# Performance work log

Measured on AMD Instinct MI355X. Metric: run time of the kernel, lower is better.

Reference implementation:

```python
import jax, jax.numpy as jnp
import numpy as np

H = 4      # num_heads
C = 64     # attention_num_c
C_Z = 128  # num_in_c (pair rep channels)
C_T = 64   # num_in_c_kv (template pair channels)


def setup_inputs() -> dict:
    key = jax.random.key(0)
    ks = jax.random.split(key, 7)
    B, T, R = 1, 4, 384
    z2d = jax.random.normal(ks[0], (B, R, R, C_Z), dtype=jnp.float32)
    t2d = jax.random.normal(ks[1], (B, T, R, R, C_T), dtype=jnp.float32)
    s = 0.02
    Wq = jax.random.normal(ks[2], (C_Z, H * C), dtype=jnp.float32) * s
    Wk = jax.random.normal(ks[3], (C_T, H * C), dtype=jnp.float32) * s
    Wv = jax.random.normal(ks[4], (C_T, H * C), dtype=jnp.float32) * s
    Wo = jax.random.normal(ks[5], (H * C, C_Z), dtype=jnp.float32) * s
    bo = jax.random.normal(ks[6], (C_Z,), dtype=jnp.float32) * s
    return {"z2d": z2d, "t2d": t2d, "Wq": Wq, "Wk": Wk, "Wv": Wv, "Wo": Wo, "bo": bo}


def reference(z2d, t2d, Wq, Wk, Wv, Wo, bo):
    B, R = z2d.shape[0], z2d.shape[-2]
    T = t2d.shape[1]
    P = R * R  # residue-pair axis
    # query: one query per residue pair
    zq = z2d.reshape(B, P, 1, C_Z)
    # templates become the key/value axis per residue pair
    tkv = jnp.transpose(t2d, (0, 2, 3, 1, 4)).reshape(B, P, T, C_T)
    q = (zq @ Wq).reshape(B, P, 1, H, C) * (C ** -0.5)
    k = (tkv @ Wk).reshape(B, P, T, H, C)
    v = (tkv @ Wv).reshape(B, P, T, H, C)
    logits = jnp.einsum('bpqhc,bpkhc->bphqk', q, k)  # [B,P,H,1,T]
    weights = jax.nn.softmax(logits, axis=-1)
    weighted_avg = jnp.einsum('bphqk,bpkhc->bpqhc', weights, v)  # [B,P,1,H,C]
    out = weighted_avg.reshape(B, P, 1, H * C) @ Wo + bo
    return out.reshape(B, R, R, C_Z)
```

## Files before the change

### kernel.cpp

```cpp
#include <hip/hip_runtime.h>


#define R_   384
#define P_   (R_ * R_)
#define NBLK (P_ / 64)

typedef __attribute__((ext_vector_type(8))) short  short8;
typedef __attribute__((ext_vector_type(4))) float  f32x4;

__device__ __forceinline__ unsigned short f2bf(float f) {
  unsigned u = __float_as_uint(f);
  unsigned r = ((u >> 16) & 1u) + 0x7FFFu;
  return (unsigned short)((u + r) >> 16);
}
__device__ __forceinline__ float bf2f(unsigned short s) {
  return __uint_as_float(((unsigned)s) << 16);
}
__device__ __forceinline__ int swz(int p, int c) {
  return p * 256 + ((((c >> 3) ^ (p & 31)) << 3) | (c & 7));
}

__global__ void prep_kernel(const float* __restrict__ Wq, const float* __restrict__ Wk,
                            const float* __restrict__ Wv, const float* __restrict__ Wo,
                            unsigned short* __restrict__ AbarT,
                            unsigned short* __restrict__ MbarT) {
  int tid = blockIdx.x * blockDim.x + threadIdx.x;
  if (tid < 256 * 128) {
    int n = tid >> 7, i = tid & 127;
    int h = n >> 6, j = n & 63;
    const float* wq = Wq + i * 256 + h * 64;
    const float* wk = Wk + j * 256 + h * 64;
    float acc = 0.f;
#pragma unroll 8
    for (int c = 0; c < 64; ++c) acc += wq[c] * wk[c];
    AbarT[n * 128 + i] = f2bf(acc * 0.125f);
  } else {
    int t2 = tid - 256 * 128;
    int o = t2 >> 8, k = t2 & 255;
    int h = k >> 6, j = k & 63;
    const float* wv = Wv + j * 256 + h * 64;
    const float* wo = Wo + (h * 64) * 128 + o;
    float acc = 0.f;
#pragma unroll 8
    for (int c = 0; c < 64; ++c) acc += wv[c] * wo[c * 128];
    MbarT[o * 256 + k] = f2bf(acc);
  }
}

__global__ __launch_bounds__(256, 2) void attn_kernel(
    const float* __restrict__ z2d, const float* __restrict__ t2d,
    const unsigned short* __restrict__ AbarT, const unsigned short* __restrict__ MbarT,
    const float* __restrict__ bo, float* __restrict__ out) {
  __shared__ __align__(16) unsigned short sT[64 * 256];
  __shared__ __align__(16) unsigned short sG[64 * 256];

  const int tid = threadIdx.x;
  const int P0  = blockIdx.x * 64;

#pragma unroll
  for (int it = 0; it < 16; ++it) {
    int f  = it * 256 + tid;
    int t  = f >> 10;
    int rr = f & 1023;
    int p  = rr >> 4;
    int j4 = (rr & 15) << 2;
    const float4 v = *(const float4*)(t2d + (size_t)(t * P_ + P0 + p) * 64 + j4);
    ushort4 pk;
    pk.x = f2bf(v.x); pk.y = f2bf(v.y); pk.z = f2bf(v.z); pk.w = f2bf(v.w);
    *(ushort4*)(sT + swz(p, t * 64 + j4)) = pk;
  }

  const int wv_  = tid >> 6;
  const int lane = tid & 63;
  const int l = lane & 15;
  const int q = lane >> 4;

  f32x4 acc[16];
#pragma unroll
  for (int i = 0; i < 16; ++i) acc[i] = f32x4{0.f, 0.f, 0.f, 0.f};
  const float* zrow = z2d + (size_t)(P0 + wv_ * 16 + l) * 128;
#pragma unroll
  for (int kk = 0; kk < 4; ++kk) {
    float4 za = *(const float4*)(zrow + kk * 32 + q * 8);
    float4 zb = *(const float4*)(zrow + kk * 32 + q * 8 + 4);
    short8 af;
    af[0] = (short)f2bf(za.x); af[1] = (short)f2bf(za.y);
    af[2] = (short)f2bf(za.z); af[3] = (short)f2bf(za.w);
    af[4] = (short)f2bf(zb.x); af[5] = (short)f2bf(zb.y);
    af[6] = (short)f2bf(zb.z); af[7] = (short)f2bf(zb.w);
    const unsigned short* bbase = AbarT + l * 128 + kk * 32 + q * 8;
#pragma unroll
    for (int nt = 0; nt < 16; ++nt) {
      short8 bf = *(const short8*)(bbase + nt * 2048);
      acc[nt] = __builtin_amdgcn_mfma_f32_16x16x32_bf16(af, bf, acc[nt], 0, 0, 0);
    }
  }
#pragma unroll
  for (int nt = 0; nt < 16; ++nt) {
    int c = nt * 16 + l;
#pragma unroll
    for (int r = 0; r < 4; ++r) {
      int p = wv_ * 16 + q * 4 + r;
      sG[swz(p, c)] = f2bf(acc[nt][r]);
    }
  }
  __syncthreads();

  {
    const int p = tid & 63;
    const int h = tid >> 6;
    float lg0 = 0.f, lg1 = 0.f, lg2 = 0.f, lg3 = 0.f;
#pragma unroll
    for (int jb = 0; jb < 64; jb += 4) {
      ushort4 g4 = *(const ushort4*)(sG + swz(p, h * 64 + jb));
      float g0 = bf2f(g4.x), g1 = bf2f(g4.y), g2 = bf2f(g4.z), g3 = bf2f(g4.w);
      ushort4 k0 = *(const ushort4*)(sT + swz(p, jb));
      ushort4 k1 = *(const ushort4*)(sT + swz(p, 64 + jb));
      ushort4 k2 = *(const ushort4*)(sT + swz(p, 128 + jb));
      ushort4 k3 = *(const ushort4*)(sT + swz(p, 192 + jb));
      lg0 += g0 * bf2f(k0.x) + g1 * bf2f(k0.y) + g2 * bf2f(k0.z) + g3 * bf2f(k0.w);
      lg1 += g0 * bf2f(k1.x) + g1 * bf2f(k1.y) + g2 * bf2f(k1.z) + g3 * bf2f(k1.w);
      lg2 += g0 * bf2f(k2.x) + g1 * bf2f(k2.y) + g2 * bf2f(k2.z) + g3 * bf2f(k2.w);
      lg3 += g0 * bf2f(k3.x) + g1 * bf2f(k3.y) + g2 * bf2f(k3.z) + g3 * bf2f(k3.w);
    }
    float mx = fmaxf(fmaxf(lg0, lg1), fmaxf(lg2, lg3));
    float e0 = __expf(lg0 - mx), e1 = __expf(lg1 - mx);
    float e2 = __expf(lg2 - mx), e3 = __expf(lg3 - mx);
    float inv = 1.f / (e0 + e1 + e2 + e3);
    e0 *= inv; e1 *= inv; e2 *= inv; e3 *= inv;
#pragma unroll
    for (int jb = 0; jb < 64; jb += 4) {
      ushort4 k0 = *(const ushort4*)(sT + swz(p, jb));
      ushort4 k1 = *(const ushort4*)(sT + swz(p, 64 + jb));
      ushort4 k2 = *(const ushort4*)(sT + swz(p, 128 + jb));
      ushort4 k3 = *(const ushort4*)(sT + swz(p, 192 + jb));
      ushort4 sv;
      sv.x = f2bf(e0 * bf2f(k0.x) + e1 * bf2f(k1.x) + e2 * bf2f(k2.x) + e3 * bf2f(k3.x));
      sv.y = f2bf(e0 * bf2f(k0.y) + e1 * bf2f(k1.y) + e2 * bf2f(k2.y) + e3 * bf2f(k3.y));
      sv.z = f2bf(e0 * bf2f(k0.z) + e1 * bf2f(k1.z) + e2 * bf2f(k2.z) + e3 * bf2f(k3.z));
      sv.w = f2bf(e0 * bf2f(k0.w) + e1 * bf2f(k1.w) + e2 * bf2f(k2.w) + e3 * bf2f(k3.w));
      *(ushort4*)(sG + swz(p, h * 64 + jb)) = sv;
    }
  }
  __syncthreads();

  f32x4 acc2[4][2];
#pragma unroll
  for (int mt = 0; mt < 4; ++mt) {
    acc2[mt][0] = f32x4{0.f, 0.f, 0.f, 0.f};
    acc2[mt][1] = f32x4{0.f, 0.f, 0.f, 0.f};
  }
#pragma unroll
  for (int kk = 0; kk < 8; ++kk) {
    const unsigned short* mb = MbarT + (size_t)(wv_ * 32 + l) * 256 + kk * 32 + q * 8;
    short8 b0 = *(const short8*)(mb);
    short8 b1 = *(const short8*)(mb + 16 * 256);
#pragma unroll
    for (int mt = 0; mt < 4; ++mt) {
      const int p  = mt * 16 + l;
      const int cb = kk * 32 + q * 8;
      short8 af2 = *(const short8*)(sG + p * 256 + (((cb >> 3) ^ (p & 31)) << 3));
      acc2[mt][0] = __builtin_amdgcn_mfma_f32_16x16x32_bf16(af2, b0, acc2[mt][0], 0, 0, 0);
      acc2[mt][1] = __builtin_amdgcn_mfma_f32_16x16x32_bf16(af2, b1, acc2[mt][1], 0, 0, 0);
    }
  }
  const float bo0 = bo[wv_ * 32 + l];
  const float bo1 = bo[wv_ * 32 + 16 + l];
#pragma unroll
  for (int mt = 0; mt < 4; ++mt) {
#pragma unroll
    for (int r = 0; r < 4; ++r) {
      size_t row = (size_t)(P0 + mt * 16 + q * 4 + r);
      out[row * 128 + wv_ * 32 + l]      = acc2[mt][0][r] + bo0;
      out[row * 128 + wv_ * 32 + 16 + l] = acc2[mt][1][r] + bo1;
    }
  }
}

extern "C" void kernel_launch(void* const* d_in, const int* in_sizes, int n_in,
                              void* d_out, int out_size, void* d_ws, size_t ws_size,
                              hipStream_t stream) {
  const float* z2d = (const float*)d_in[0];
  const float* t2d = (const float*)d_in[1];
  const float* Wq  = (const float*)d_in[2];
  const float* Wk  = (const float*)d_in[3];
  const float* Wv  = (const float*)d_in[4];
  const float* Wo  = (const float*)d_in[5];
  const float* bo  = (const float*)d_in[6];

  unsigned short* AbarT = (unsigned short*)d_ws;
  unsigned short* MbarT = AbarT + 256 * 128;
  float* out = (float*)d_out;

  hipLaunchKernelGGL(prep_kernel, dim3(256), dim3(256), 0, stream,
                     Wq, Wk, Wv, Wo, AbarT, MbarT);
  hipLaunchKernelGGL(attn_kernel, dim3(NBLK), dim3(256), 0, stream,
                     z2d, t2d, AbarT, MbarT, bo, out);
}
```

Before: 358.3 us.

## Halve attention tile to 32 pairs, re-split waves, and rewrite weight prep with LDS

The attention kernel now processes 32 residue pairs per block instead of 64, halving shared memory and accumulator registers, and raises launch bounds to 4 blocks per CU. Waves are re-split into an M-tile by N-half grid for both MFMA GEMMs, and the logit/softmax stage splits each pair's channel reduction across two threads combined with a shuffle. The weight-folding prep kernel is rewritten to stage Wq/Wk/Wv/Wo slices in padded shared memory with 8 blocks instead of 256 strided-global-load blocks. The smaller tile increases redundant loads of the folded weight matrices per pair and doubles block count.

```diff
diff --git a/kernel.cpp b/kernel.cpp
--- a/kernel.cpp
+++ b/kernel.cpp
@@ -3,7 +3,7 @@
 
 #define R_   384
 #define P_   (R_ * R_)
-#define NBLK (P_ / 64)
+#define NBLK (P_ / 32)
 
 typedef __attribute__((ext_vector_type(8))) short  short8;
 typedef __attribute__((ext_vector_type(4))) float  f32x4;
@@ -24,44 +24,75 @@
                             const float* __restrict__ Wv, const float* __restrict__ Wo,
                             unsigned short* __restrict__ AbarT,
                             unsigned short* __restrict__ MbarT) {
-  int tid = blockIdx.x * blockDim.x + threadIdx.x;
-  if (tid < 256 * 128) {
-    int n = tid >> 7, i = tid & 127;
-    int h = n >> 6, j = n & 63;
-    const float* wq = Wq + i * 256 + h * 64;
-    const float* wk = Wk + j * 256 + h * 64;
-    float acc = 0.f;
+  __shared__ float sA[128 * 65];
+  __shared__ float sB[64 * 65];
+  const int t = threadIdx.x;
+  if (blockIdx.x < 4) {
+    const int h = blockIdx.x;
+    for (int it = 0; it < 8; ++it) {
+      int idx = it * 256 + t;
+      int row = idx >> 4, c4 = (idx & 15) << 2;
+      float4 v = *(const float4*)(Wq + row * 256 + h * 64 + c4);
+      sA[row * 65 + c4 + 0] = v.x; sA[row * 65 + c4 + 1] = v.y;
+      sA[row * 65 + c4 + 2] = v.z; sA[row * 65 + c4 + 3] = v.w;
+    }
+    for (int it = 0; it < 4; ++it) {
+      int idx = it * 256 + t;
+      int row = idx >> 4, c4 = (idx & 15) << 2;
+      float4 v = *(const float4*)(Wk + row * 256 + h * 64 + c4);
+      sB[row * 65 + c4 + 0] = v.x; sB[row * 65 + c4 + 1] = v.y;
+      sB[row * 65 + c4 + 2] = v.z; sB[row * 65 + c4 + 3] = v.w;
+    }
+    __syncthreads();
+    const int i = t & 127, jh2 = t >> 7;
+    for (int jj = 0; jj < 32; ++jj) {
+      int j = jh2 * 32 + jj;
+      float acc = 0.f;
 #pragma unroll 8
-    for (int c = 0; c < 64; ++c) acc += wq[c] * wk[c];
-    AbarT[n * 128 + i] = f2bf(acc * 0.125f);
+      for (int c = 0; c < 64; ++c) acc += sA[i * 65 + c] * sB[j * 65 + c];
+      AbarT[(h * 64 + j) * 128 + i] = f2bf(acc * 0.125f);
+    }
   } else {
-    int t2 = tid - 256 * 128;
-    int o = t2 >> 8, k = t2 & 255;
-    int h = k >> 6, j = k & 63;
-    const float* wv = Wv + j * 256 + h * 64;
-    const float* wo = Wo + (h * 64) * 128 + o;
-    float acc = 0.f;
+    const int h = blockIdx.x - 4;
+    for (int it = 0; it < 8; ++it) {
+      int idx = it * 256 + t;
+      int row = idx >> 5, o4 = (idx & 31) << 2;
+      *(float4*)(sA + row * 128 + o4) = *(const float4*)(Wo + (h * 64 + row) * 128 + o4);
+    }
+    for (int it = 0; it < 4; ++it) {
+      int idx = it * 256 + t;
+      int row = idx >> 4, c4 = (idx & 15) << 2;
+      float4 v = *(const float4*)(Wv + row * 256 + h * 64 + c4);
+      sB[row * 65 + c4 + 0] = v.x; sB[row * 65 + c4 + 1] = v.y;
+      sB[row * 65 + c4 + 2] = v.z; sB[row * 65 + c4 + 3] = v.w;
+    }
+    __syncthreads();
+    const int o = t & 127, jh2 = t >> 7;
+    for (int jj = 0; jj < 32; ++jj) {
+      int j = jh2 * 32 + jj;
+      float acc = 0.f;
 #pragma unroll 8
-    for (int c = 0; c < 64; ++c) acc += wv[c] * wo[c * 128];
-    MbarT[o * 256 + k] = f2bf(acc);
-  }
-}
-
-__global__ __launch_bounds__(256, 2) void attn_kernel(
+      for (int c = 0; c < 64; ++c) acc += sB[j * 65 + c] * sA[c * 128 + o];
+      MbarT[o * 256 + h * 64 + j] = f2bf(acc);
+    }
+  }
+}
+
+__global__ __launch_bounds__(256, 4) void attn_kernel(
     const float* __restrict__ z2d, const float* __restrict__ t2d,
     const unsigned short* __restrict__ AbarT, const unsigned short* __restrict__ MbarT,
     const float* __restrict__ bo, float* __restrict__ out) {
-  __shared__ __align__(16) unsigned short sT[64 * 256];
-  __shared__ __align__(16) unsigned short sG[64 * 256];
+  __shared__ __align__(16) unsigned short sT[32 * 256];
+  __shared__ __align__(16) unsigned short sG[32 * 256];
 
   const int tid = threadIdx.x;
-  const int P0  = blockIdx.x * 64;
-
-#pragma unroll
-  for (int it = 0; it < 16; ++it) {
+  const int P0  = blockIdx.x * 32;
+
+#pragma unroll
+  for (int it = 0; it < 8; ++it) {
     int f  = it * 256 + tid;
-    int t  = f >> 10;
-    int rr = f & 1023;
+    int t  = f >> 9;
+    int rr = f & 511;
     int p  = rr >> 4;
     int j4 = (rr & 15) << 2;
     const float4 v = *(const float4*)(t2d + (size_t)(t * P_ + P0 + p) * 64 + j4);
@@ -71,14 +102,16 @@
   }
 
   const int wv_  = tid >> 6;
+  const int mt   = wv_ >> 1;
+  const int nh   = wv_ & 1;
   const int lane = tid & 63;
   const int l = lane & 15;
   const int q = lane >> 4;
 
-  f32x4 acc[16];
-#pragma unroll
-  for (int i = 0; i < 16; ++i) acc[i] = f32x4{0.f, 0.f, 0.f, 0.f};
-  const float* zrow = z2d + (size_t)(P0 + wv_ * 16 + l) * 128;
+  f32x4 acc[8];
+#pragma unroll
+  for (int i = 0; i < 8; ++i) acc[i] = f32x4{0.f, 0.f, 0.f, 0.f};
+  const float* zrow = z2d + (size_t)(P0 + mt * 16 + l) * 128;
 #pragma unroll
   for (int kk = 0; kk < 4; ++kk) {
     float4 za = *(const float4*)(zrow + kk * 32 + q * 8);
@@ -88,91 +121,92 @@
     af[2] = (short)f2bf(za.z); af[3] = (short)f2bf(za.w);
     af[4] = (short)f2bf(zb.x); af[5] = (short)f2bf(zb.y);
     af[6] = (short)f2bf(zb.z); af[7] = (short)f2bf(zb.w);
-    const unsigned short* bbase = AbarT + l * 128 + kk * 32 + q * 8;
-#pragma unroll
-    for (int nt = 0; nt < 16; ++nt) {
+    const unsigned short* bbase = AbarT + (size_t)(nh * 128 + l) * 128 + kk * 32 + q * 8;
+#pragma unroll
+    for (int nt = 0; nt < 8; ++nt) {
       short8 bf = *(const short8*)(bbase + nt * 2048);
       acc[nt] = __builtin_amdgcn_mfma_f32_16x16x32_bf16(af, bf, acc[nt], 0, 0, 0);
     }
   }
 #pragma unroll
-  for (int nt = 0; nt < 16; ++nt) {
-    int c = nt * 16 + l;
+  for (int nt = 0; nt < 8; ++nt) {
+    int c = nh * 128 + nt * 16 + l;
 #pragma unroll
     for (int r = 0; r < 4; ++r) {
-      int p = wv_ * 16 + q * 4 + r;
+      int p = mt * 16 + q * 4 + r;
       sG[swz(p, c)] = f2bf(acc[nt][r]);
     }
   }
   __syncthreads();
 
   {
-    const int p = tid & 63;
-    const int h = tid >> 6;
+    const int jh = tid & 1;
+    const int p  = (tid >> 1) & 31;
+    const int h  = tid >> 6;
+    const int c0 = h * 64 + jh * 32;
+    const int t0 = jh * 32;
     float lg0 = 0.f, lg1 = 0.f, lg2 = 0.f, lg3 = 0.f;
 #pragma unroll
-    for (int jb = 0; jb < 64; jb += 4) {
-      ushort4 g4 = *(const ushort4*)(sG + swz(p, h * 64 + jb));
+    for (int jb = 0; jb < 32; jb += 4) {
+      ushort4 g4 = *(const ushort4*)(sG + swz(p, c0 + jb));
       float g0 = bf2f(g4.x), g1 = bf2f(g4.y), g2 = bf2f(g4.z), g3 = bf2f(g4.w);
-      ushort4 k0 = *(const ushort4*)(sT + swz(p, jb));
-      ushort4 k1 = *(const ushort4*)(sT + swz(p, 64 + jb));
-      ushort4 k2 = *(const ushort4*)(sT + swz(p, 128 + jb));
-      ushort4 k3 = *(const ushort4*)(sT + swz(p, 192 + jb));
+      ushort4 k0 = *(const ushort4*)(sT + swz(p, t0 + jb));
+      ushort4 k1 = *(const ushort4*)(sT + swz(p, 64 + t0 + jb));
+      ushort4 k2 = *(const ushort4*)(sT + swz(p, 128 + t0 + jb));
+      ushort4 k3 = *(const ushort4*)(sT + swz(p, 192 + t0 + jb));
       lg0 += g0 * bf2f(k0.x) + g1 * bf2f(k0.y) + g2 * bf2f(k0.z) + g3 * bf2f(k0.w);
       lg1 += g0 * bf2f(k1.x) + g1 * bf2f(k1.y) + g2 * bf2f(k1.z) + g3 * bf2f(k1.w);
       lg2 += g0 * bf2f(k2.x) + g1 * bf2f(k2.y) + g2 * bf2f(k2.z) + g3 * bf2f(k2.w);
       lg3 += g0 * bf2f(k3.x) + g1 * bf2f(k3.y) + g2 * bf2f(k3.z) + g3 * bf2f(k3.w);
     }
+    lg0 += __shfl_xor(lg0, 1);
+    lg1 += __shfl_xor(lg1, 1);
+    lg2 += __shfl_xor(lg2, 1);
+    lg3 += __shfl_xor(lg3, 1);
     float mx = fmaxf(fmaxf(lg0, lg1), fmaxf(lg2, lg3));
     float e0 = __expf(lg0 - mx), e1 = __expf(lg1 - mx);
     float e2 = __expf(lg2 - mx), e3 = __expf(lg3 - mx);
     float inv = 1.f / (e0 + e1 + e2 + e3);
     e0 *= inv; e1 *= inv; e2 *= inv; e3 *= inv;
 #pragma unroll
-    for (int jb = 0; jb < 64; jb += 4) {
-      ushort4 k0 = *(const ushort4*)(sT + swz(p, jb));
-      ushort4 k1 = *(const ushort4*)(sT + swz(p, 64 + jb));
-      ushort4 k2 = *(const ushort4*)(sT + swz(p, 128 + jb));
-      ushort4 k3 = *(const ushort4*)(sT + swz(p, 192 + jb));
+    for (int jb = 0; jb < 32; jb += 4) {
+      ushort4 k0 = *(const ushort4*)(sT + swz(p, t0 + jb));
+      ushort4 k1 = *(const ushort4*)(sT + swz(p, 64 + t0 + jb));
+      ushort4 k2 = *(const ushort4*)(sT + swz(p, 128 + t0 + jb));
+      ushort4 k3 = *(const ushort4*)(sT + swz(p, 192 + t0 + jb));
       ushort4 sv;
       sv.x = f2bf(e0 * bf2f(k0.x) + e1 * bf2f(k1.x) + e2 * bf2f(k2.x) + e3 * bf2f(k3.x));
       sv.y = f2bf(e0 * bf2f(k0.y) + e1 * bf2f(k1.y) + e2 * bf2f(k2.y) + e3 * bf2f(k3.y));
       sv.z = f2bf(e0 * bf2f(k0.z) + e1 * bf2f(k1.z) + e2 * bf2f(k2.z) + e3 * bf2f(k3.z));
       sv.w = f2bf(e0 * bf2f(k0.w) + e1 * bf2f(k1.w) + e2 * bf2f(k2.w) + e3 * bf2f(k3.w));
-      *(ushort4*)(sG + swz(p, h * 64 + jb)) = sv;
+      *(ushort4*)(sG + swz(p, c0 + jb)) = sv;
     }
   }
   __syncthreads();
 
-  f32x4 acc2[4][2];
-#pragma unroll
-  for (int mt = 0; mt < 4; ++mt) {
-    acc2[mt][0] = f32x4{0.f, 0.f, 0.f, 0.f};
-    acc2[mt][1] = f32x4{0.f, 0.f, 0.f, 0.f};
-  }
+  f32x4 acc2[4];
+#pragma unroll
+  for (int nt = 0; nt < 4; ++nt) acc2[nt] = f32x4{0.f, 0.f, 0.f, 0.f};
 #pragma unroll
   for (int kk = 0; kk < 8; ++kk) {
-    const unsigned short* mb = MbarT + (size_t)(wv_ * 32 + l) * 256 + kk * 32 + q * 8;
-    short8 b0 = *(const short8*)(mb);
-    short8 b1 = *(const short8*)(mb + 16 * 256);
-#pragma unroll
-    for (int mt = 0; mt < 4; ++mt) {
-      const int p  = mt * 16 + l;
-      const int cb = kk * 32 + q * 8;
-      short8 af2 = *(const short8*)(sG + p * 256 + (((cb >> 3) ^ (p & 31)) << 3));
-      acc2[mt][0] = __builtin_amdgcn_mfma_f32_16x16x32_bf16(af2, b0, acc2[mt][0], 0, 0, 0);
-      acc2[mt][1] = __builtin_amdgcn_mfma_f32_16x16x32_bf16(af2, b1, acc2[mt][1], 0, 0, 0);
-    }
-  }
-  const float bo0 = bo[wv_ * 32 + l];
-  const float bo1 = bo[wv_ * 32 + 16 + l];
-#pragma unroll
-  for (int mt = 0; mt < 4; ++mt) {
+    const int cb = kk * 32 + q * 8;
+    const int p  = mt * 16 + l;
+    short8 af2 = *(const short8*)(sG + p * 256 + (((cb >> 3) ^ (p & 31)) << 3));
+    const unsigned short* mb = MbarT + (size_t)(nh * 64 + l) * 256 + cb;
+#pragma unroll
+    for (int nt = 0; nt < 4; ++nt) {
+      short8 bf = *(const short8*)(mb + nt * 4096);
+      acc2[nt] = __builtin_amdgcn_mfma_f32_16x16x32_bf16(af2, bf, acc2[nt], 0, 0, 0);
+    }
+  }
+#pragma unroll
+  for (int nt = 0; nt < 4; ++nt) {
+    const int col = nh * 64 + nt * 16 + l;
+    const float b = bo[col];
 #pragma unroll
     for (int r = 0; r < 4; ++r) {
       size_t row = (size_t)(P0 + mt * 16 + q * 4 + r);
-      out[row * 128 + wv_ * 32 + l]      = acc2[mt][0][r] + bo0;
-      out[row * 128 + wv_ * 32 + 16 + l] = acc2[mt][1][r] + bo1;
+      out[row * 128 + col] = acc2[nt][r] + b;
     }
   }
 }
@@ -192,7 +226,7 @@
   unsigned short* MbarT = AbarT + 256 * 128;
   float* out = (float*)d_out;
 
-  hipLaunchKernelGGL(prep_kernel, dim3(256), dim3(256), 0, stream,
+  hipLaunchKernelGGL(prep_kernel, dim3(8), dim3(256), 0, stream,
                      Wq, Wk, Wv, Wo, AbarT, MbarT);
   hipLaunchKernelGGL(attn_kernel, dim3(NBLK), dim3(256), 0, stream,
                      z2d, t2d, AbarT, MbarT, bo, out);
```

Result: slower. 421.2 us (+17.6%).
